# Kernel tuning notes

Measured on AMD Instinct MI355X. Metric: run time of the kernel, lower is better.

Reference implementation:

```python
import jax, jax.numpy as jnp
import numpy as np

N, E = 50000, 400000
D_IN, D_H, N_CLS = 256, 64, 50
BN_EPS = 1e-5


def _gat_layer(x, src, dst, W, att_s, att_d, bias, heads, out_c, concat):
    # x: [N, in]; W: [in, heads*out_c]; att_s/att_d: [heads, out_c]
    n = x.shape[0]
    h = (x @ W).reshape(n, heads, out_c)                       # [N,H,C]
    a_s = jnp.einsum('nhc,hc->nh', h, att_s)                   # [N,H]
    a_d = jnp.einsum('nhc,hc->nh', h, att_d)
    e = jax.nn.leaky_relu(a_s[src] + a_d[dst], 0.2)            # [E',H]
    emax = jax.lax.stop_gradient(jax.ops.segment_max(e, dst, num_segments=n))
    emax = jnp.where(jnp.isfinite(emax), emax, 0.0)
    p = jnp.exp(e - emax[dst])
    denom = jax.ops.segment_sum(p, dst, num_segments=n)
    alpha = p / (denom[dst] + 1e-16)                           # segment softmax over in-edges of dst
    out = jax.ops.segment_sum(h[src] * alpha[:, :, None], dst, num_segments=n)  # [N,H,C]
    out = out.reshape(n, heads * out_c) if concat else out.mean(axis=1)
    return out + bias


def _bn_eval(x, g, b, rm, rv):
    return (x - rm) * g * jax.lax.rsqrt(rv + BN_EPS) + b


def setup_inputs() -> dict:
    key = jax.random.key(0)
    ks = jax.random.split(key, 24)
    s = lambda i, shape: jax.random.normal(ks[i], shape, dtype=jnp.float32) * 0.05
    inp = {
        'x': jax.random.normal(ks[0], (N, D_IN), dtype=jnp.float32),
        'edge_index': jax.random.randint(ks[1], (2, E), 0, N, dtype=jnp.int64),
        # GAT layer 1: heads=8, concat=False
        'W1': s(2, (D_IN, 8 * D_H)), 'as1': s(3, (8, D_H)), 'ad1': s(4, (8, D_H)), 'b1': s(5, (D_H,)),
        # GAT layer 2: heads=4, concat=False
        'W2': s(6, (D_H, 4 * D_H)), 'as2': s(7, (4, D_H)), 'ad2': s(8, (4, D_H)), 'b2': s(9, (D_H,)),
        # GAT layer 3: heads=1, concat=True
        'W3': s(10, (D_H, D_H)), 'as3': s(11, (1, D_H)), 'ad3': s(12, (1, D_H)), 'b3': s(13, (D_H,)),
        # BatchNorm (eval mode, running stats)
        'bn1_g': jnp.ones((D_H,), jnp.float32), 'bn1_b': jnp.zeros((D_H,), jnp.float32),
        'bn1_m': s(14, (D_H,)), 'bn1_v': jax.random.uniform(ks[15], (D_H,), jnp.float32) + 0.5,
        'bn2_g': jnp.ones((D_H,), jnp.float32), 'bn2_b': jnp.zeros((D_H,), jnp.float32),
        'bn2_m': s(16, (D_H,)), 'bn2_v': jax.random.uniform(ks[17], (D_H,), jnp.float32) + 0.5,
        # topic classifier
        'cW1': s(18, (D_H, D_H)), 'cb1': s(19, (D_H,)),
        'cW2': s(20, (D_H, N_CLS)), 'cb2': s(21, (N_CLS,)),
    }
    return inp


def reference(x, edge_index, W1, as1, ad1, b1, W2, as2, ad2, b2, W3, as3, ad3, b3,
              bn1_g, bn1_b, bn1_m, bn1_v, bn2_g, bn2_b, bn2_m, bn2_v,
              cW1, cb1, cW2, cb2):
    n = x.shape[0]
    loops = jnp.arange(n, dtype=edge_index.dtype)
    src = jnp.concatenate([edge_index[0], loops])   # add_self_loops=True (PyG default)
    dst = jnp.concatenate([edge_index[1], loops])

    h = _gat_layer(x, src, dst, W1, as1, ad1, b1, heads=8, out_c=D_H, concat=False)
    h = jax.nn.relu(_bn_eval(h, bn1_g, bn1_b, bn1_m, bn1_v))
    h = _gat_layer(h, src, dst, W2, as2, ad2, b2, heads=4, out_c=D_H, concat=False)
    h = jax.nn.relu(_bn_eval(h, bn2_g, bn2_b, bn2_m, bn2_v))
    h = _gat_layer(h, src, dst, W3, as3, ad3, b3, heads=1, out_c=D_H, concat=True)

    z = jax.nn.relu(h @ cW1 + cb1)
    logits = z @ cW2 + cb2
    return jax.nn.softmax(logits, axis=-1)
```

## Files before the change

kernel.cpp:

```cpp
#include <hip/hip_runtime.h>
#include <hip/hip_bf16.h>
#include <math.h>

#define NN 50000
#define EE 400000
#define D_IN 256
#define D_H 64
#define N_CLS 50

typedef __attribute__((ext_vector_type(8))) short bfrag;
typedef __attribute__((ext_vector_type(4))) float ffrag;
typedef __attribute__((ext_vector_type(8))) unsigned short u16x8_t;
typedef __attribute__((ext_vector_type(4))) unsigned short u16x4_t;

__device__ __forceinline__ unsigned short f2bf(float v) {
    unsigned int u = __float_as_uint(v);
    unsigned int r = (u + 0x7fffu + ((u >> 16) & 1u)) >> 16;
    return (unsigned short)r;
}
__device__ __forceinline__ float bf2f(unsigned short b) {
    return __uint_as_float(((unsigned int)b) << 16);
}

__device__ __forceinline__ int swz(int row, int q) {
    return row * 32 + ((q ^ ((row >> 1) & 3)) << 3);
}

__global__ void count_k(const int* __restrict__ ei, int* __restrict__ cnt, int E, int N) {
    int i = blockIdx.x * blockDim.x + threadIdx.x;
    if (i >= E + N) return;
    int dst = (i < E) ? ei[E + i] : (i - E);
    atomicAdd(&cnt[dst], 1);
}

__global__ __launch_bounds__(1024) void scan1_k(const int* __restrict__ counts,
                                                int* __restrict__ excl,
                                                int* __restrict__ bsum, int n) {
    __shared__ int wsum[16];
    int t = threadIdx.x;
    int lane = t & 63, wid = t >> 6;
    int idx = blockIdx.x * 1024 + t;
    int v = (idx < n) ? counts[idx] : 0;
    int incl = v;
    #pragma unroll
    for (int off = 1; off < 64; off <<= 1) {
        int x = __shfl_up(incl, off);
        if (lane >= off) incl += x;
    }
    if (lane == 63) wsum[wid] = incl;
    __syncthreads();
    if (wid == 0) {
        int ws = (lane < 16) ? wsum[lane] : 0;
        int wincl = ws;
        #pragma unroll
        for (int off = 1; off < 16; off <<= 1) {
            int x = __shfl_up(wincl, off);
            if (lane >= off) wincl += x;
        }
        if (lane < 16) wsum[lane] = wincl - ws;
    }
    __syncthreads();
    if (idx < n) excl[idx] = wsum[wid] + (incl - v);
    if (t == 1023) bsum[blockIdx.x] = wsum[15] + incl;
}

__global__ void scan2_k(int* __restrict__ bsum, int nb) {
    int lane = threadIdx.x & 63;
    int v = (lane < nb) ? bsum[lane] : 0;
    int incl = v;
    #pragma unroll
    for (int off = 1; off < 64; off <<= 1) {
        int x = __shfl_up(incl, off);
        if (lane >= off) incl += x;
    }
    if (lane < nb) bsum[lane] = incl - v;
}

__global__ void scan3_k(const int* __restrict__ excl, const int* __restrict__ bsum,
                        int* __restrict__ rowptr, int n, int total) {
    int i = blockIdx.x * 256 + threadIdx.x;
    if (i < n) rowptr[i] = excl[i] + bsum[i >> 10];
    if (i == 0) rowptr[n] = total;
}

__global__ void fill_k(const int* __restrict__ ei, const int* __restrict__ rowptr,
                       int* __restrict__ cursor, int* __restrict__ csr, int E, int N) {
    int i = blockIdx.x * blockDim.x + threadIdx.x;
    if (i >= E + N) return;
    int s, d;
    if (i < E) { s = ei[i]; d = ei[E + i]; }
    else       { s = i - E; d = i - E; }
    int pos = atomicAdd(&cursor[d], 1);
    csr[rowptr[d] + pos] = s;
}

__global__ __launch_bounds__(64) void prep_k(
    const float* __restrict__ W3, const float* __restrict__ cW1,
    const float* __restrict__ as3, const float* __restrict__ ad3,
    const float* __restrict__ b3, const float* __restrict__ cb1,
    const float* __restrict__ bn1g, const float* __restrict__ bn1b,
    const float* __restrict__ bn1m, const float* __restrict__ bn1v,
    const float* __restrict__ b1,
    const float* __restrict__ bn2g, const float* __restrict__ bn2b,
    const float* __restrict__ bn2m, const float* __restrict__ bn2v,
    const float* __restrict__ b2,
    float* __restrict__ Wc, float* __restrict__ w_as3,
    float* __restrict__ w_ad3, float* __restrict__ bc,
    float* __restrict__ sc1, float* __restrict__ sh1,
    float* __restrict__ sc2, float* __restrict__ sh2) {
    int bj = blockIdx.x;
    int i = threadIdx.x;
    if (bj < 64) {
        int j = bj;
        float s = 0.f;
        for (int k = 0; k < 64; k++) s += W3[i * 64 + k] * cW1[k * 64 + j];
        Wc[i * 64 + j] = s;
        if (j == 0) {
            float sa = 0.f, sd = 0.f;
            for (int c = 0; c < 64; c++) {
                sa += W3[i * 64 + c] * as3[c];
                sd += W3[i * 64 + c] * ad3[c];
            }
            w_as3[i] = sa;
            w_ad3[i] = sd;
        }
        if (i == 0) {
            float s2 = 0.f;
            for (int k = 0; k < 64; k++) s2 += b3[k] * cW1[k * 64 + j];
            bc[j] = s2 + cb1[j];
        }
    } else if (bj == 64) {
        float sc = bn1g[i] * rsqrtf(bn1v[i] + 1e-5f);
        sc1[i] = sc;
        sh1[i] = (b1[i] - bn1m[i]) * sc + bn1b[i];
    } else {
        float sc = bn2g[i] * rsqrtf(bn2v[i] + 1e-5f);
        sc2[i] = sc;
        sh2[i] = (b2[i] - bn2m[i]) * sc + bn2b[i];
    }
}

#define S_W1 131072
#define S_W2 (S_W1 + 16384)
#define S_WC (S_W2 + 4096)
#define S_WL (S_WC + 3200)
__global__ void cvt_all_k(
    const float* __restrict__ W1, const float* __restrict__ W2,
    const float* __restrict__ Wc, const float* __restrict__ cW2,
    unsigned short* __restrict__ w1h, unsigned short* __restrict__ w1l,
    unsigned short* __restrict__ w2h, unsigned short* __restrict__ w2l,
    unsigned short* __restrict__ wch, unsigned short* __restrict__ wcl,
    unsigned short* __restrict__ wlh, unsigned short* __restrict__ wll) {
    int i = blockIdx.x * 256 + threadIdx.x;
    const float* src; unsigned short* dh; unsigned short* dl;
    int K, Nn, j;
    if (i < S_W1)      { j = i;        src = W1;  dh = w1h; dl = w1l; K = 256; Nn = 512; }
    else if (i < S_W2) { j = i - S_W1; src = W2;  dh = w2h; dl = w2l; K = 64;  Nn = 256; }
    else if (i < S_WC) { j = i - S_W2; src = Wc;  dh = wch; dl = wcl; K = 64;  Nn = 64;  }
    else if (i < S_WL) { j = i - S_WC; src = cW2; dh = wlh; dl = wll; K = 64;  Nn = 50;  }
    else return;
    int k = j / Nn, n = j - k * Nn;
    float v = src[j];
    unsigned short h = f2bf(v);
    dh[(size_t)n * K + k] = h;
    dl[(size_t)n * K + k] = f2bf(v - bf2f(h));
}

__global__ __launch_bounds__(256) void gemm_mfma_k(
    const float* __restrict__ Af,
    const unsigned short* __restrict__ Ahi, const unsigned short* __restrict__ Alo,
    const unsigned short* __restrict__ BThi, const unsigned short* __restrict__ BTlo,
    float* __restrict__ Cf, unsigned short* __restrict__ Chi, unsigned short* __restrict__ Clo,
    int M, int N, int K,
    const float* __restrict__ bias, int do_relu,
    const float* __restrict__ att_s, const float* __restrict__ att_d,
    float* __restrict__ asb, float* __restrict__ adb, int H) {
    __shared__ unsigned short sAh[64 * 32];
    __shared__ unsigned short sAl[64 * 32];
    __shared__ unsigned short sBh[128 * 32];
    __shared__ unsigned short sBl[128 * 32];
    const int tid = threadIdx.x;
    const int m0 = blockIdx.y * 64;
    const int n0 = blockIdx.x * 128;
    const int lane = tid & 63, w = tid >> 6;
    const int wm = w >> 1, wn = w & 1;
    const int c16 = lane & 15, kq = lane >> 4;
    const int arow = tid >> 2;
    const int q    = tid & 3;
    const int akc  = q * 8;
    const int aM  = min(m0 + arow, M - 1);
    const int bn0 = min(n0 + arow, N - 1);
    const int bn1 = min(n0 + 64 + arow, N - 1);
    const int wA  = swz(arow, q);
    const int wB0 = swz(arow, q);
    const int wB1 = swz(64 + arow, q);
    const float* pAf          = Af  ? Af  + (size_t)aM * K + akc : nullptr;
    const unsigned short* pAh = Ahi ? Ahi + (size_t)aM * K + akc : nullptr;
    const unsigned short* pAl = Alo ? Alo + (size_t)aM * K + akc : nullptr;
    const unsigned short* pBh0 = BThi + (size_t)bn0 * K + akc;
    const unsigned short* pBl0 = BTlo + (size_t)bn0 * K + akc;
    const unsigned short* pBh1 = BThi + (size_t)bn1 * K + akc;
    const unsigned short* pBl1 = BTlo + (size_t)bn1 * K + akc;
    ffrag acc[2][4] = {};

    for (int k0 = 0; k0 < K; k0 += 32) {
        bfrag va_h, va_l;
        if (Af) {
            float4 f0 = *(const float4*)(pAf + k0);
            float4 f1 = *(const float4*)(pAf + k0 + 4);
            float fv[8] = {f0.x, f0.y, f0.z, f0.w, f1.x, f1.y, f1.z, f1.w};
            #pragma unroll
            for (int i = 0; i < 8; i++) {
                unsigned short hh = f2bf(fv[i]);
                va_h[i] = (short)hh;
                va_l[i] = (short)f2bf(fv[i] - bf2f(hh));
            }
        } else {
            va_h = *(const bfrag*)(pAh + k0);
            va_l = *(const bfrag*)(pAl + k0);
        }
        bfrag vb_h0 = *(const bfrag*)(pBh0 + k0);
        bfrag vb_l0 = *(const bfrag*)(pBl0 + k0);
        bfrag vb_h1 = *(const bfrag*)(pBh1 + k0);
        bfrag vb_l1 = *(const bfrag*)(pBl1 + k0);
        __syncthreads();
        *(bfrag*)&sAh[wA]  = va_h;
        *(bfrag*)&sAl[wA]  = va_l;
        *(bfrag*)&sBh[wB0] = vb_h0;
        *(bfrag*)&sBl[wB0] = vb_l0;
        *(bfrag*)&sBh[wB1] = vb_h1;
        *(bfrag*)&sBl[wB1] = vb_l1;
        __syncthreads();
        bfrag ah[2], al_[2], bh[4], bl[4];
        #pragma unroll
        for (int mt = 0; mt < 2; mt++) {
            int ra = wm * 32 + mt * 16 + c16;
            ah[mt]  = *(const bfrag*)&sAh[swz(ra, kq)];
            al_[mt] = *(const bfrag*)&sAl[swz(ra, kq)];
        }
        #pragma unroll
        for (int nt = 0; nt < 4; nt++) {
            int rb = wn * 64 + nt * 16 + c16;
            bh[nt] = *(const bfrag*)&sBh[swz(rb, kq)];
            bl[nt] = *(const bfrag*)&sBl[swz(rb, kq)];
        }
        #pragma unroll
        for (int mt = 0; mt < 2; mt++)
            #pragma unroll
            for (int nt = 0; nt < 4; nt++) {
                acc[mt][nt] = __builtin_amdgcn_mfma_f32_16x16x32_bf16(ah[mt],  bh[nt], acc[mt][nt], 0, 0, 0);
                acc[mt][nt] = __builtin_amdgcn_mfma_f32_16x16x32_bf16(ah[mt],  bl[nt], acc[mt][nt], 0, 0, 0);
                acc[mt][nt] = __builtin_amdgcn_mfma_f32_16x16x32_bf16(al_[mt], bh[nt], acc[mt][nt], 0, 0, 0);
            }
    }

    if (att_s) {
        int hidx = n0 / 64 + wn;
        if (hidx < H) {
            float s_att[4], d_att[4];
            #pragma unroll
            for (int nt = 0; nt < 4; nt++) {
                s_att[nt] = att_s[hidx * 64 + nt * 16 + c16];
                d_att[nt] = att_d[hidx * 64 + nt * 16 + c16];
            }
            #pragma unroll
            for (int mt = 0; mt < 2; mt++) {
                #pragma unroll
                for (int r = 0; r < 4; r++) {
                    int row = m0 + wm * 32 + mt * 16 + kq * 4 + r;
                    float ps = 0.f, pd = 0.f;
                    #pragma unroll
                    for (int nt = 0; nt < 4; nt++) {
                        ps = fmaf(acc[mt][nt][r], s_att[nt], ps);
                        pd = fmaf(acc[mt][nt][r], d_att[nt], pd);
                    }
                    #pragma unroll
                    for (int msk = 1; msk < 16; msk <<= 1) {
                        ps += __shfl_xor(ps, msk);
                        pd += __shfl_xor(pd, msk);
                    }
                    if (c16 == 0 && row < M) {
                        asb[(size_t)row * H + hidx] = ps;
                        adb[(size_t)row * H + hidx] = pd;
                    }
                }
            }
        }
    }

    #pragma unroll
    for (int mt = 0; mt < 2; mt++) {
        #pragma unroll
        for (int r = 0; r < 4; r++) {
            int row = m0 + wm * 32 + mt * 16 + kq * 4 + r;
            if (row < M) {
                #pragma unroll
                for (int nt = 0; nt < 4; nt++) {
                    int col = n0 + wn * 64 + nt * 16 + c16;
                    if (col < N) {
                        float v = acc[mt][nt][r];
                        if (bias) v += bias[col];
                        if (do_relu) v = fmaxf(v, 0.f);
                        size_t idx = (size_t)row * N + col;
                        if (Cf) Cf[idx] = v;
                        if (Chi) {
                            unsigned short hh = f2bf(v);
                            Chi[idx] = hh;
                            if (Clo) Clo[idx] = f2bf(v - bf2f(hh));
                        }
                    }
                }
            }
        }
    }
}

__device__ __forceinline__ float wave_max_f(float v) {
    #pragma unroll
    for (int off = 32; off; off >>= 1) v = fmaxf(v, __shfl_xor(v, off));
    return v;
}
__device__ __forceinline__ float wave_sum_f(float v) {
    #pragma unroll
    for (int off = 32; off; off >>= 1) v += __shfl_xor(v, off);
    return v;
}

template <int H, bool MEAN_BN>
__global__ __launch_bounds__(256) void agg_k(
    const unsigned short* __restrict__ hfeat,
    const float* __restrict__ a_s, const float* __restrict__ a_d,
    const int* __restrict__ rowptr, const int* __restrict__ csr,
    const float* __restrict__ scale,
    const float* __restrict__ shift,
    unsigned short* __restrict__ outhi, unsigned short* __restrict__ outlo,
    const float* __restrict__ was3, const float* __restrict__ wad3,
    float* __restrict__ as3o, float* __restrict__ ad3o,
    int N) {
    constexpr int OUT = H * 64;
    constexpr int F = H;
    constexpr int G = 64 / H;
    constexpr int EPC = 64 / H;
    __shared__ float alpha_s[4][H][65];
    __shared__ int srcb[4][64];
    const int wv = threadIdx.x >> 6;
    const int lane = threadIdx.x & 63;
    const int node = blockIdx.x * 4 + wv;
    if (node >= N) return;

    const int row = rowptr[node];
    const int deg = rowptr[node + 1] - row;
    const int hl = lane / G;

    float acc[F] = {};
    float inv = 1.f;

    if (deg <= 64) {
        const int j8 = lane / H;
        const int h8 = lane % H;
        float adn_own = a_d[(size_t)node * H + h8];
        float psum = 0.f;
        for (int c0 = 0; c0 < deg; c0 += EPC) {
            int jj = c0 + j8;
            if (jj < deg) {
                int s = csr[row + jj];
                if (h8 == 0) srcb[wv][jj] = s;
                float e = a_s[(size_t)s * H + h8] + adn_own;
                e = e > 0.f ? e : 0.2f * e;
                float p = __expf(e);
                alpha_s[wv][h8][jj] = p;
                psum += p;
            }
        }
        #pragma unroll
        for (int msk = H; msk < 64; msk <<= 1)
            psum += __shfl_xor(psum, msk);
        float invd = 1.f / (psum + 1e-16f);
        inv = __shfl(invd, hl);
        asm volatile("s_waitcnt lgkmcnt(0)" ::: "memory");
        for (int jj = 0; jj < deg; jj++) {
            int ss = srcb[wv][jj];
            float al = alpha_s[wv][hl][jj];
            const unsigned short* rp = hfeat + (size_t)ss * OUT + lane * F;
            if constexpr (F == 8) {
                u16x8_t u = *(const u16x8_t*)rp;
                #pragma unroll
                for (int i = 0; i < 8; i++) acc[i] = fmaf(al, bf2f(u[i]), acc[i]);
            } else if constexpr (F == 4) {
                u16x4_t u = *(const u16x4_t*)rp;
                #pragma unroll
                for (int i = 0; i < 4; i++) acc[i] = fmaf(al, bf2f(u[i]), acc[i]);
            } else {
                acc[0] = fmaf(al, bf2f(rp[0]), acc[0]);
            }
        }
    } else {
        float adn[H];
        #pragma unroll
        for (int h = 0; h < H; h++) adn[h] = a_d[(size_t)node * H + h];
        float m[H];
        #pragma unroll
        for (int h = 0; h < H; h++) m[h] = -INFINITY;
        for (int c0 = 0; c0 < deg; c0 += 64) {
            int j = c0 + lane;
            if (j < deg) {
                int s2 = csr[row + j];
                #pragma unroll
                for (int h = 0; h < H; h++) {
                    float e = a_s[(size_t)s2 * H + h] + adn[h];
                    e = e > 0.f ? e : 0.2f * e;
                    m[h] = fmaxf(m[h], e);
                }
            }
        }
        #pragma unroll
        for (int h = 0; h < H; h++) m[h] = wave_max_f(m[h]);
        float dsum[H] = {};
        for (int c0 = 0; c0 < deg; c0 += 64) {
            int j = c0 + lane;
            if (j < deg) {
                int s2 = csr[row + j];
                #pragma unroll
                for (int h = 0; h < H; h++) {
                    float e = a_s[(size_t)s2 * H + h] + adn[h];
                    e = e > 0.f ? e : 0.2f * e;
                    dsum[h] += __expf(e - m[h]);
                }
            }
        }
        float dinv[H];
        #pragma unroll
        for (int h = 0; h < H; h++) dinv[h] = 1.f / (wave_sum_f(dsum[h]) + 1e-16f);
        for (int c0 = 0; c0 < deg; c0 += 64) {
            int j = c0 + lane;
            int cnt = min(64, deg - c0);
            int s = 0;
            if (j < deg) {
                s = csr[row + j];
                #pragma unroll
                for (int h = 0; h < H; h++) {
                    float e = a_s[(size_t)s * H + h] + adn[h];
                    e = e > 0.f ? e : 0.2f * e;
                    alpha_s[wv][h][lane] = __expf(e - m[h]) * dinv[h];
                }
            }
            asm volatile("s_waitcnt lgkmcnt(0)" ::: "memory");
            for (int jj = 0; jj < cnt; jj++) {
                int ss = __builtin_amdgcn_readlane(s, jj);
                float al = alpha_s[wv][hl][jj];
                const unsigned short* rp = hfeat + (size_t)ss * OUT + lane * F;
                if constexpr (F == 8) {
                    u16x8_t u = *(const u16x8_t*)rp;
                    #pragma unroll
                    for (int i = 0; i < 8; i++) acc[i] = fmaf(al, bf2f(u[i]), acc[i]);
                } else if constexpr (F == 4) {
                    u16x4_t u = *(const u16x4_t*)rp;
                    #pragma unroll
                    for (int i = 0; i < 4; i++) acc[i] = fmaf(al, bf2f(u[i]), acc[i]);
                } else {
                    acc[0] = fmaf(al, bf2f(rp[0]), acc[0]);
                }
            }
            asm volatile("s_waitcnt lgkmcnt(0)" ::: "memory");
        }
        inv = 1.f;
    }

    #pragma unroll
    for (int i = 0; i < F; i++) acc[i] *= inv;

    if constexpr (MEAN_BN) {
        #pragma unroll
        for (int i = 0; i < F; i++) {
            #pragma unroll
            for (int msk = G; msk < 64; msk <<= 1)
                acc[i] += __shfl_xor(acc[i], msk);
        }
        const int c0 = (lane < G) ? lane * F : 0;
        float res[F];
        if (lane < G) {
            #pragma unroll
            for (int i = 0; i < F; i++) {
                float v = fmaf(acc[i] * (1.0f / H), scale[c0 + i], shift[c0 + i]);
                res[i] = fmaxf(v, 0.f);
            }
        } else {
            #pragma unroll
            for (int i = 0; i < F; i++) res[i] = 0.f;
        }
        if (was3) {
            float ps = 0.f, pd = 0.f;
            if (lane < G) {
                #pragma unroll
                for (int i = 0; i < F; i++) {
                    ps = fmaf(res[i], was3[c0 + i], ps);
                    pd = fmaf(res[i], wad3[c0 + i], pd);
                }
            }
            #pragma unroll
            for (int msk = 1; msk < G; msk <<= 1) {
                ps += __shfl_xor(ps, msk);
                pd += __shfl_xor(pd, msk);
            }
            if (lane == 0) { as3o[node] = ps; ad3o[node] = pd; }
        }
        if (lane < G) {
            #pragma unroll
            for (int i = 0; i < F; i++) {
                unsigned short hh = f2bf(res[i]);
                outhi[(size_t)node * 64 + c0 + i] = hh;
                if (outlo) outlo[(size_t)node * 64 + c0 + i] = f2bf(res[i] - bf2f(hh));
            }
        }
    } else {
        float v = acc[0] + (shift ? shift[lane] : 0.f);
        unsigned short hh = f2bf(v);
        outhi[(size_t)node * 64 + lane] = hh;
        if (outlo) outlo[(size_t)node * 64 + lane] = f2bf(v - bf2f(hh));
    }
}

__global__ __launch_bounds__(256) void softmax_k(const float* __restrict__ logits,
                                                 float* __restrict__ out, int N) {
    int lane = threadIdx.x & 63;
    int n = (blockIdx.x * blockDim.x + threadIdx.x) >> 6;
    if (n >= N) return;
    float lg = (lane < N_CLS) ? logits[(size_t)n * N_CLS + lane] : -INFINITY;
    float m = wave_max_f(lg);
    float p = (lane < N_CLS) ? __expf(lg - m) : 0.f;
    float s = wave_sum_f(p);
    if (lane < N_CLS) out[(size_t)n * N_CLS + lane] = p / s;
}

extern "C" void kernel_launch(void* const* d_in, const int* in_sizes, int n_in,
                              void* d_out, int out_size, void* d_ws, size_t ws_size,
                              hipStream_t stream) {
    const int N = NN, E = EE, E2 = EE + NN;
    const float* x    = (const float*)d_in[0];
    const int*   ei   = (const int*)d_in[1];
    const float* W1   = (const float*)d_in[2];
    const float* as1  = (const float*)d_in[3];
    const float* ad1  = (const float*)d_in[4];
    const float* b1   = (const float*)d_in[5];
    const float* W2   = (const float*)d_in[6];
    const float* as2  = (const float*)d_in[7];
    const float* ad2  = (const float*)d_in[8];
    const float* b2   = (const float*)d_in[9];
    const float* W3   = (const float*)d_in[10];
    const float* as3  = (const float*)d_in[11];
    const float* ad3  = (const float*)d_in[12];
    const float* b3   = (const float*)d_in[13];
    const float* bn1g = (const float*)d_in[14];
    const float* bn1b = (const float*)d_in[15];
    const float* bn1m = (const float*)d_in[16];
    const float* bn1v = (const float*)d_in[17];
    const float* bn2g = (const float*)d_in[18];
    const float* bn2b = (const float*)d_in[19];
    const float* bn2m = (const float*)d_in[20];
    const float* bn2v = (const float*)d_in[21];
    const float* cW1  = (const float*)d_in[22];
    const float* cb1  = (const float*)d_in[23];
    const float* cW2  = (const float*)d_in[24];
    const float* cb2  = (const float*)d_in[25];
    float* out = (float*)d_out;

    char* ws = (char*)d_ws;
    size_t off = 0;
    auto alloc = [&](size_t bytes) {
        void* p = ws + off;
        off = (off + bytes + 255) & ~(size_t)255;
        return p;
    };
    int*   rowptr = (int*)alloc((size_t)(N + 1) * 4);
    int*   cursor = (int*)alloc((size_t)N * 4);
    int*   excl   = (int*)alloc((size_t)N * 4);
    int*   bsum   = (int*)alloc(64 * 4);
    int*   csr    = (int*)alloc((size_t)E2 * 4);
    unsigned short* hbf = (unsigned short*)alloc((size_t)N * 512 * 2);
    float* asb    = (float*)alloc((size_t)N * 8 * 4);
    float* adb    = (float*)alloc((size_t)N * 8 * 4);
    float* as3b   = (float*)alloc((size_t)N * 4);
    float* ad3b   = (float*)alloc((size_t)N * 4);
    unsigned short* f1h = (unsigned short*)alloc((size_t)N * 64 * 2);
    unsigned short* f1l = (unsigned short*)alloc((size_t)N * 64 * 2);
    unsigned short* f2h = (unsigned short*)alloc((size_t)N * 64 * 2);
    unsigned short* f3h = (unsigned short*)alloc((size_t)N * 64 * 2);
    unsigned short* f3l = (unsigned short*)alloc((size_t)N * 64 * 2);
    unsigned short* zh  = (unsigned short*)alloc((size_t)N * 64 * 2);
    unsigned short* zl  = (unsigned short*)alloc((size_t)N * 64 * 2);
    unsigned short* w1h = (unsigned short*)alloc((size_t)S_W1 * 2);
    unsigned short* w1l = (unsigned short*)alloc((size_t)S_W1 * 2);
    unsigned short* w2h = (unsigned short*)alloc(16384 * 2);
    unsigned short* w2l = (unsigned short*)alloc(16384 * 2);
    unsigned short* wch = (unsigned short*)alloc(4096 * 2);
    unsigned short* wcl = (unsigned short*)alloc(4096 * 2);
    unsigned short* wlh = (unsigned short*)alloc(3200 * 2);
    unsigned short* wll = (unsigned short*)alloc(3200 * 2);
    float* sc1 = (float*)alloc(64 * 4);
    float* sh1 = (float*)alloc(64 * 4);
    float* sc2 = (float*)alloc(64 * 4);
    float* sh2 = (float*)alloc(64 * 4);
    float* Wc    = (float*)alloc(64 * 64 * 4);
    float* w_as3 = (float*)alloc(64 * 4);
    float* w_ad3 = (float*)alloc(64 * 4);
    float* bc    = (float*)alloc(64 * 4);
    float* logits = (float*)alloc((size_t)N * N_CLS * 4);

    const int NB = (N + 1023) / 1024;

    hipMemsetAsync(cursor, 0, (size_t)N * 4, stream);
    count_k<<<(E2 + 255) / 256, 256, 0, stream>>>(ei, cursor, E, N);
    scan1_k<<<NB, 1024, 0, stream>>>(cursor, excl, bsum, N);
    scan2_k<<<1, 64, 0, stream>>>(bsum, NB);
    scan3_k<<<(N + 255) / 256, 256, 0, stream>>>(excl, bsum, rowptr, N, E2);
    hipMemsetAsync(cursor, 0, (size_t)N * 4, stream);
    fill_k<<<(E2 + 255) / 256, 256, 0, stream>>>(ei, rowptr, cursor, csr, E, N);
    prep_k<<<66, 64, 0, stream>>>(W3, cW1, as3, ad3, b3, cb1,
                                  bn1g, bn1b, bn1m, bn1v, b1,
                                  bn2g, bn2b, bn2m, bn2v, b2,
                                  Wc, w_as3, w_ad3, bc, sc1, sh1, sc2, sh2);
    cvt_all_k<<<(S_WL + 255) / 256, 256, 0, stream>>>(W1, W2, Wc, cW2,
        w1h, w1l, w2h, w2l, wch, wcl, wlh, wll);

    const int MB = (N + 63) / 64;
    const int AB = (N + 3) / 4;

    gemm_mfma_k<<<dim3(4, MB), 256, 0, stream>>>(x, nullptr, nullptr, w1h, w1l,
        nullptr, hbf, nullptr, N, 512, 256, nullptr, 0, as1, ad1, asb, adb, 8);
    agg_k<8, true><<<AB, 256, 0, stream>>>(hbf, asb, adb, rowptr, csr, sc1, sh1,
        f1h, f1l, nullptr, nullptr, nullptr, nullptr, N);

    gemm_mfma_k<<<dim3(2, MB), 256, 0, stream>>>(nullptr, f1h, f1l, w2h, w2l,
        nullptr, hbf, nullptr, N, 256, 64, nullptr, 0, as2, ad2, asb, adb, 4);
    agg_k<4, true><<<AB, 256, 0, stream>>>(hbf, asb, adb, rowptr, csr, sc2, sh2,
        f2h, nullptr, w_as3, w_ad3, as3b, ad3b, N);

    agg_k<1, false><<<AB, 256, 0, stream>>>(f2h, as3b, ad3b, rowptr, csr, nullptr, nullptr,
        f3h, f3l, nullptr, nullptr, nullptr, nullptr, N);
    gemm_mfma_k<<<dim3(1, MB), 256, 0, stream>>>(nullptr, f3h, f3l, wch, wcl,
        nullptr, zh, zl, N, 64, 64, bc, 1, nullptr, nullptr, nullptr, nullptr, 0);

    gemm_mfma_k<<<dim3(1, MB), 256, 0, stream>>>(nullptr, zh, zl, wlh, wll,
        logits, nullptr, nullptr, N, N_CLS, 64, cb2, 0, nullptr, nullptr, nullptr, nullptr, 0);
    softmax_k<<<(N + 3) / 4, 256, 0, stream>>>(logits, out, N);
}
```

Measured before the change: 455.4 us.

## Fuse classifier GEMMs and softmax into one kernel

Replaces the two classifier GEMM launches and the separate softmax kernel with a single kernel. The hidden activation stays in shared memory, where it is split into bf16 hi/lo parts for the second MFMA GEMM, and the softmax is applied in registers using 16-lane shuffles. This removes the global round-trips for the z and logits buffers and two kernel launches. In exchange, each block reads its B fragments straight from global memory without LDS staging.

```diff
diff --git a/kernel.cpp b/kernel.cpp
--- a/kernel.cpp
+++ b/kernel.cpp
@@ -315,6 +315,101 @@
     }
 }
 
+__global__ __launch_bounds__(256) void cls_fused_k(
+    const unsigned short* __restrict__ Ah, const unsigned short* __restrict__ Al,
+    const unsigned short* __restrict__ Bh1, const unsigned short* __restrict__ Bl1,
+    const float* __restrict__ bias1,
+    const unsigned short* __restrict__ Bh2, const unsigned short* __restrict__ Bl2,
+    const float* __restrict__ bias2,
+    float* __restrict__ out, int M) {
+    __shared__ float zs[64][65];
+    const int tid = threadIdx.x;
+    const int lane = tid & 63, w = tid >> 6;
+    const int c16 = lane & 15, kq = lane >> 4;
+    const int m0 = blockIdx.x * 64;
+    const int arow = min(m0 + w * 16 + c16, M - 1);
+
+    ffrag acc1[4] = {};
+    #pragma unroll
+    for (int kit = 0; kit < 2; kit++) {
+        int kb = kit * 32 + kq * 8;
+        bfrag ah  = *(const bfrag*)(Ah + (size_t)arow * 64 + kb);
+        bfrag al_ = *(const bfrag*)(Al + (size_t)arow * 64 + kb);
+        #pragma unroll
+        for (int nt = 0; nt < 4; nt++) {
+            int bcol = nt * 16 + c16;
+            bfrag bh = *(const bfrag*)(Bh1 + (size_t)bcol * 64 + kb);
+            bfrag bl = *(const bfrag*)(Bl1 + (size_t)bcol * 64 + kb);
+            acc1[nt] = __builtin_amdgcn_mfma_f32_16x16x32_bf16(ah,  bh, acc1[nt], 0, 0, 0);
+            acc1[nt] = __builtin_amdgcn_mfma_f32_16x16x32_bf16(ah,  bl, acc1[nt], 0, 0, 0);
+            acc1[nt] = __builtin_amdgcn_mfma_f32_16x16x32_bf16(al_, bh, acc1[nt], 0, 0, 0);
+        }
+    }
+    #pragma unroll
+    for (int nt = 0; nt < 4; nt++)
+        #pragma unroll
+        for (int r = 0; r < 4; r++) {
+            int row = w * 16 + kq * 4 + r;
+            int col = nt * 16 + c16;
+            zs[row][col] = fmaxf(acc1[nt][r] + bias1[col], 0.f);
+        }
+    __syncthreads();
+
+    ffrag acc2[4] = {};
+    #pragma unroll
+    for (int kit = 0; kit < 2; kit++) {
+        int kb = kit * 32 + kq * 8;
+        float fv[8];
+        #pragma unroll
+        for (int i = 0; i < 8; i++) fv[i] = zs[w * 16 + c16][kb + i];
+        bfrag ah, al_;
+        #pragma unroll
+        for (int i = 0; i < 8; i++) {
+            unsigned short hh = f2bf(fv[i]);
+            ah[i]  = (short)hh;
+            al_[i] = (short)f2bf(fv[i] - bf2f(hh));
+        }
+        #pragma unroll
+        for (int nt = 0; nt < 4; nt++) {
+            int bcol = min(nt * 16 + c16, N_CLS - 1);
+            bfrag bh = *(const bfrag*)(Bh2 + (size_t)bcol * 64 + kb);
+            bfrag bl = *(const bfrag*)(Bl2 + (size_t)bcol * 64 + kb);
+            acc2[nt] = __builtin_amdgcn_mfma_f32_16x16x32_bf16(ah,  bh, acc2[nt], 0, 0, 0);
+            acc2[nt] = __builtin_amdgcn_mfma_f32_16x16x32_bf16(ah,  bl, acc2[nt], 0, 0, 0);
+            acc2[nt] = __builtin_amdgcn_mfma_f32_16x16x32_bf16(al_, bh, acc2[nt], 0, 0, 0);
+        }
+    }
+    #pragma unroll
+    for (int r = 0; r < 4; r++) {
+        int row = m0 + w * 16 + kq * 4 + r;
+        float lg[4], mx = -INFINITY;
+        #pragma unroll
+        for (int nt = 0; nt < 4; nt++) {
+            int col = nt * 16 + c16;
+            lg[nt] = (col < N_CLS) ? acc2[nt][r] + bias2[col] : -INFINITY;
+            mx = fmaxf(mx, lg[nt]);
+        }
+        #pragma unroll
+        for (int msk = 1; msk < 16; msk <<= 1) mx = fmaxf(mx, __shfl_xor(mx, msk));
+        float p[4], ps = 0.f;
+        #pragma unroll
+        for (int nt = 0; nt < 4; nt++) {
+            p[nt] = (nt * 16 + c16 < N_CLS) ? __expf(lg[nt] - mx) : 0.f;
+            ps += p[nt];
+        }
+        #pragma unroll
+        for (int msk = 1; msk < 16; msk <<= 1) ps += __shfl_xor(ps, msk);
+        float invs = 1.f / ps;
+        if (row < M) {
+            #pragma unroll
+            for (int nt = 0; nt < 4; nt++) {
+                int col = nt * 16 + c16;
+                if (col < N_CLS) out[(size_t)row * N_CLS + col] = p[nt] * invs;
+            }
+        }
+    }
+}
+
 __device__ __forceinline__ float wave_max_f(float v) {
     #pragma unroll
     for (int off = 32; off; off >>= 1) v = fmaxf(v, __shfl_xor(v, off));
@@ -518,18 +613,6 @@
         outhi[(size_t)node * 64 + lane] = hh;
         if (outlo) outlo[(size_t)node * 64 + lane] = f2bf(v - bf2f(hh));
     }
-}
-
-__global__ __launch_bounds__(256) void softmax_k(const float* __restrict__ logits,
-                                                 float* __restrict__ out, int N) {
-    int lane = threadIdx.x & 63;
-    int n = (blockIdx.x * blockDim.x + threadIdx.x) >> 6;
-    if (n >= N) return;
-    float lg = (lane < N_CLS) ? logits[(size_t)n * N_CLS + lane] : -INFINITY;
-    float m = wave_max_f(lg);
-    float p = (lane < N_CLS) ? __expf(lg - m) : 0.f;
-    float s = wave_sum_f(p);
-    if (lane < N_CLS) out[(size_t)n * N_CLS + lane] = p / s;
 }
 
 extern "C" void kernel_launch(void* const* d_in, const int* in_sizes, int n_in,
@@ -586,10 +669,8 @@
     unsigned short* f2h = (unsigned short*)alloc((size_t)N * 64 * 2);
     unsigned short* f3h = (unsigned short*)alloc((size_t)N * 64 * 2);
     unsigned short* f3l = (unsigned short*)alloc((size_t)N * 64 * 2);
-    unsigned short* zh  = (unsigned short*)alloc((size_t)N * 64 * 2);
-    unsigned short* zl  = (unsigned short*)alloc((size_t)N * 64 * 2);
-    unsigned short* w1h = (unsigned short*)alloc((size_t)S_W1 * 2);
-    unsigned short* w1l = (unsigned short*)alloc((size_t)S_W1 * 2);
+    unsigned short* w1h = (unsigned short*)alloc((size_t)131072 * 2);
+    unsigned short* w1l = (unsigned short*)alloc((size_t)131072 * 2);
     unsigned short* w2h = (unsigned short*)alloc(16384 * 2);
     unsigned short* w2l = (unsigned short*)alloc(16384 * 2);
     unsigned short* wch = (unsigned short*)alloc(4096 * 2);
@@ -604,7 +685,6 @@
     float* w_as3 = (float*)alloc(64 * 4);
     float* w_ad3 = (float*)alloc(64 * 4);
     float* bc    = (float*)alloc(64 * 4);
-    float* logits = (float*)alloc((size_t)N * N_CLS * 4);
 
     const int NB = (N + 1023) / 1024;
 
@@ -637,10 +717,6 @@
 
     agg_k<1, false><<<AB, 256, 0, stream>>>(f2h, as3b, ad3b, rowptr, csr, nullptr, nullptr,
         f3h, f3l, nullptr, nullptr, nullptr, nullptr, N);
-    gemm_mfma_k<<<dim3(1, MB), 256, 0, stream>>>(nullptr, f3h, f3l, wch, wcl,
-        nullptr, zh, zl, N, 64, 64, bc, 1, nullptr, nullptr, nullptr, nullptr, 0);
-
-    gemm_mfma_k<<<dim3(1, MB), 256, 0, stream>>>(nullptr, zh, zl, wlh, wll,
-        logits, nullptr, nullptr, N, N_CLS, 64, cb2, 0, nullptr, nullptr, nullptr, nullptr, 0);
-    softmax_k<<<(N + 3) / 4, 256, 0, stream>>>(logits, out, N);
-}
+
+    cls_fused_k<<<MB, 256, 0, stream>>>(f3h, f3l, wch, wcl, bc, wlh, wll, cb2, out, N);
+}
```

Measured after the change: 439.2 us. 1.04x faster.
